# Kernel optimization log

Measured on AMD Instinct MI355X. Metric: run time of the kernel, lower is better.

The kernel has to match this reference:

```python
import jax, jax.numpy as jnp
import numpy as np

HIDDEN = 2048
KEY = 2048
EPS = 1e-05


def setup_inputs() -> dict:
    key = jax.random.key(0)
    k1, k2, k3 = jax.random.split(key, 3)
    B, S = 4, 2048
    x = jax.random.normal(k1, (B, S, HIDDEN), dtype=jnp.float32)
    # kaiming_uniform_ bound for fan_in=HIDDEN (a=sqrt(5) default): sqrt(6/((1+5)*fan_in)) = 1/sqrt(fan_in)
    bq = 1.0 / np.sqrt(HIDDEN)
    qkv = jax.random.uniform(k2, (HIDDEN, KEY * 3), minval=-bq, maxval=bq, dtype=jnp.float32)
    bo = 1.0 / np.sqrt(KEY)
    o_proj = jax.random.uniform(k3, (KEY, HIDDEN), minval=-bo, maxval=bo, dtype=jnp.float32)
    gamma = jnp.ones((HIDDEN,), dtype=jnp.float32)
    beta = jnp.zeros((HIDDEN,), dtype=jnp.float32)
    return {"x": x, "qkv": qkv, "o_proj": o_proj, "gamma": gamma, "beta": beta}


def reference(x, qkv, o_proj, gamma, beta):
    residual = x
    # LayerNorm over last dim
    mu = jnp.mean(x, axis=-1, keepdims=True)
    var = jnp.mean((x - mu) ** 2, axis=-1, keepdims=True)
    x_norm = (x - mu) / jnp.sqrt(var + EPS) * gamma + beta
    q = x_norm @ qkv[:, :KEY]          # [B,S,K]
    k = x_norm @ qkv[:, KEY:2 * KEY]   # [B,S,K]
    v = x_norm @ qkv[:, 2 * KEY:]      # [B,S,K]
    scale = 1.0 / jnp.sqrt(jnp.float32(KEY))
    scores = jnp.einsum('bsk,btk->bst', q, k) * scale  # [B,S,S]
    S_len = x.shape[1]
    causal = jnp.tril(jnp.ones((S_len, S_len), dtype=bool))
    scores = jnp.where(causal[None], scores, -jnp.inf)
    attn = jax.nn.softmax(scores, axis=-1)
    out = attn @ v          # [B,S,K]
    out = out @ o_proj      # [B,S,H]
    return out + residual
```

## Files before the change

### kernel.cpp

```cpp
#include <hip/hip_runtime.h>
#include <stdint.h>

typedef short short8 __attribute__((ext_vector_type(8)));
typedef unsigned short ushort8 __attribute__((ext_vector_type(8)));
typedef unsigned short ushort4v __attribute__((ext_vector_type(4)));
typedef float f32x4 __attribute__((ext_vector_type(4)));

#define HD 2048
#define S_LEN 2048
#define NROWS 8192
#define N3 6144

typedef __attribute__((address_space(3))) void lds_void_t;
typedef __attribute__((address_space(1))) void g_void_t;

__device__ inline void gload_lds16(const void* g, void* l) {
    __builtin_amdgcn_global_load_lds((g_void_t*)g, (lds_void_t*)l, 16, 0, 0);
}

__device__ inline unsigned short f2bf(float f) {
    unsigned u = __float_as_uint(f);
    unsigned r = (u + 0x7FFFu + ((u >> 16) & 1u)) >> 16;
    return (unsigned short)r;
}
__device__ inline float bf2f(unsigned short h) {
    return __uint_as_float(((unsigned)h) << 16);
}

__global__ __launch_bounds__(256) void ln_kernel(const float* __restrict__ x,
    const float* __restrict__ gamma, const float* __restrict__ beta,
    unsigned short* __restrict__ xn) {
    int row = blockIdx.x;
    const float* xr = x + (size_t)row * HD;
    int tid = threadIdx.x;
    float v[8];
    float4 a = *(const float4*)(xr + tid * 8);
    float4 b = *(const float4*)(xr + tid * 8 + 4);
    v[0]=a.x; v[1]=a.y; v[2]=a.z; v[3]=a.w; v[4]=b.x; v[5]=b.y; v[6]=b.z; v[7]=b.w;
    float s = 0.f, ss = 0.f;
#pragma unroll
    for (int e = 0; e < 8; e++) { s += v[e]; ss += v[e] * v[e]; }
    for (int off = 32; off > 0; off >>= 1) {
        s += __shfl_down(s, off);
        ss += __shfl_down(ss, off);
    }
    __shared__ float red[10];
    int wave = tid >> 6, lane = tid & 63;
    if (lane == 0) { red[wave] = s; red[4 + wave] = ss; }
    __syncthreads();
    if (tid == 0) {
        float S = red[0] + red[1] + red[2] + red[3];
        float SS = red[4] + red[5] + red[6] + red[7];
        float mu = S * (1.0f / HD);
        float var = SS * (1.0f / HD) - mu * mu;
        red[8] = mu;
        red[9] = rsqrtf(var + 1e-5f);
    }
    __syncthreads();
    float mu = red[8], rstd = red[9];
#pragma unroll
    for (int e = 0; e < 8; e++) {
        int c = tid * 8 + e;
        float val = (v[e] - mu) * rstd * gamma[c] + beta[c];
        xn[(size_t)row * HD + c] = f2bf(val);
    }
}

__global__ __launch_bounds__(256) void transp_f32_bf16(const float* __restrict__ src, int ld_s,
    unsigned short* __restrict__ dst, int ld_d) {
    __shared__ float tile[32][33];
    int c0 = blockIdx.x * 32, r0 = blockIdx.y * 32;
    int tc = threadIdx.x & 31, tr = threadIdx.x >> 5;
#pragma unroll
    for (int i = 0; i < 32; i += 8)
        tile[tr + i][tc] = src[(size_t)(r0 + tr + i) * ld_s + c0 + tc];
    __syncthreads();
#pragma unroll
    for (int i = 0; i < 32; i += 8)
        dst[(size_t)(c0 + tr + i) * ld_d + r0 + tc] = f2bf(tile[tc][tr + i]);
}

__global__ __launch_bounds__(256) void softmax_causal(unsigned short* __restrict__ sc) {
    int r = blockIdx.x;
    int s = r & (S_LEN - 1);
    unsigned short* row = sc + (size_t)r * S_LEN;
    int tid = threadIdx.x;
    ushort8 u = *(const ushort8*)(row + tid * 8);
    float v[8];
    float mx = -3.0e38f;
#pragma unroll
    for (int e = 0; e < 8; e++) {
        int t = tid * 8 + e;
        float f = bf2f(u[e]);
        v[e] = (t <= s) ? f : -3.0e38f;
        mx = fmaxf(mx, v[e]);
    }
    for (int off = 32; off > 0; off >>= 1) mx = fmaxf(mx, __shfl_down(mx, off));
    __shared__ float red[8];
    int wave = tid >> 6, lane = tid & 63;
    if (lane == 0) red[wave] = mx;
    __syncthreads();
    mx = fmaxf(fmaxf(red[0], red[1]), fmaxf(red[2], red[3]));
    float ex[8];
    float sum = 0.f;
#pragma unroll
    for (int e = 0; e < 8; e++) {
        ex[e] = (v[e] > -1.0e38f) ? __expf(v[e] - mx) : 0.f;
        sum += ex[e];
    }
    for (int off = 32; off > 0; off >>= 1) sum += __shfl_down(sum, off);
    if (lane == 0) red[4 + wave] = sum;
    __syncthreads();
    float inv = 1.0f / (red[4] + red[5] + red[6] + red[7]);
#pragma unroll
    for (int e = 0; e < 8; e++) {
        row[tid * 8 + e] = f2bf(ex[e] * inv);
    }
}

template <int EPI>
__global__ __launch_bounds__(256) void gemm_nt(
    const unsigned short* __restrict__ Ab, int lda, long sAz,
    const unsigned short* __restrict__ Bb, int ldb, long sBz,
    void* __restrict__ Cb, int ldc, long sCz,
    int kdim, int causal, float scale, const float* __restrict__ resid,
    unsigned short* __restrict__ vt) {
    int bx = blockIdx.x, by = blockIdx.y, bz = blockIdx.z;
    if (causal) by = gridDim.y - 1 - by;
    if (causal == 1 && bx > by) return;
    const unsigned short* A = Ab + (size_t)bz * sAz;
    const unsigned short* Bt = Bb + (size_t)bz * sBz;
    int kmax = kdim;
    if (causal == 2) { int km = (by + 1) * 128; if (km < kmax) kmax = km; }
    int m0 = by * 128, n0 = bx * 128;

    __shared__ unsigned short lA[128 * 64];
    __shared__ unsigned short lB[128 * 64];

    int tid = threadIdx.x;
    int wave = tid >> 6, lane = tid & 63;
    int quad = lane >> 4, l16 = lane & 15;
    int wr = wave >> 1, wc = wave & 1;

    int rstage = wave * 32 + (lane >> 2);
    int ck = (lane & 3) * 8;
    const unsigned short* gA[2][2];
    const unsigned short* gB[2][2];
    unsigned short* ldA[2][2];
    unsigned short* ldB[2][2];
#pragma unroll
    for (int r16 = 0; r16 < 2; r16++)
#pragma unroll
        for (int h = 0; h < 2; h++) {
            gA[r16][h] = A + (size_t)(m0 + rstage + r16 * 16) * lda + h * 32 + ck;
            gB[r16][h] = Bt + (size_t)(n0 + rstage + r16 * 16) * ldb + h * 32 + ck;
            ldA[r16][h] = &lA[h * 4096 + (wave * 32 + r16 * 16) * 32];
            ldB[r16][h] = &lB[h * 4096 + (wave * 32 + r16 * 16) * 32];
        }

    f32x4 acc[4][4] = {};

    for (int k0 = 0; k0 < kmax; k0 += 64) {
        __syncthreads();
#pragma unroll
        for (int r16 = 0; r16 < 2; r16++)
#pragma unroll
            for (int h = 0; h < 2; h++) {
                gload_lds16(gA[r16][h], ldA[r16][h]);
                gload_lds16(gB[r16][h], ldB[r16][h]);
            }
        __syncthreads();
#pragma unroll
        for (int h = 0; h < 2; h++) {
            short8 af[4], bfr[4];
#pragma unroll
            for (int i = 0; i < 4; i++)
                af[i] = *(const short8*)&lA[h * 4096 + (wr * 64 + i * 16 + l16) * 32 + quad * 8];
#pragma unroll
            for (int j = 0; j < 4; j++)
                bfr[j] = *(const short8*)&lB[h * 4096 + (wc * 64 + j * 16 + l16) * 32 + quad * 8];
#pragma unroll
            for (int i = 0; i < 4; i++)
#pragma unroll
                for (int j = 0; j < 4; j++)
                    acc[i][j] = __builtin_amdgcn_mfma_f32_16x16x32_bf16(af[i], bfr[j], acc[i][j], 0, 0, 0);
        }
#pragma unroll
        for (int r16 = 0; r16 < 2; r16++)
#pragma unroll
            for (int h = 0; h < 2; h++) { gA[r16][h] += 64; gB[r16][h] += 64; }
    }

    int row0 = m0 + wr * 64 + quad * 4;
    int col0 = n0 + wc * 64 + l16;
    if (EPI == 3 && n0 >= 4096) {
        int batch = m0 >> 11;
        int sl0 = (m0 & 2047) + wr * 64 + quad * 4;
#pragma unroll
        for (int j = 0; j < 4; j++) {
            int kcol = (n0 - 4096) + wc * 64 + j * 16 + l16;
            unsigned short* base = vt + (size_t)batch * S_LEN * S_LEN + (size_t)kcol * S_LEN + sl0;
#pragma unroll
            for (int i = 0; i < 4; i++) {
                ushort4v p;
#pragma unroll
                for (int r = 0; r < 4; r++) p[r] = f2bf(acc[i][j][r]);
                *(ushort4v*)(base + i * 16) = p;
            }
        }
    } else if (EPI == 0 || EPI == 1 || EPI == 3) {
        unsigned short* C = (unsigned short*)Cb + (size_t)bz * sCz;
#pragma unroll
        for (int i = 0; i < 4; i++)
#pragma unroll
            for (int r = 0; r < 4; r++) {
                int row = row0 + i * 16 + r;
#pragma unroll
                for (int j = 0; j < 4; j++) {
                    float v = acc[i][j][r];
                    if (EPI == 1) v *= scale;
                    C[(size_t)row * ldc + col0 + j * 16] = f2bf(v);
                }
            }
    } else {
        float* C = (float*)Cb + (size_t)bz * sCz;
#pragma unroll
        for (int i = 0; i < 4; i++)
#pragma unroll
            for (int r = 0; r < 4; r++) {
                int row = row0 + i * 16 + r;
#pragma unroll
                for (int j = 0; j < 4; j++) {
                    int col = col0 + j * 16;
                    C[(size_t)row * ldc + col] = acc[i][j][r] + resid[(size_t)row * ldc + col];
                }
            }
    }
}

extern "C" void kernel_launch(void* const* d_in, const int* in_sizes, int n_in,
                              void* d_out, int out_size, void* d_ws, size_t ws_size,
                              hipStream_t stream) {
    const float* x      = (const float*)d_in[0];
    const float* qkv    = (const float*)d_in[1];
    const float* o_proj = (const float*)d_in[2];
    const float* gamma  = (const float*)d_in[3];
    const float* beta   = (const float*)d_in[4];
    float* out = (float*)d_out;

    char* w = (char*)d_ws;
    unsigned short* xn      = (unsigned short*)(w);
    unsigned short* w_t     = (unsigned short*)(w + 33554432);
    unsigned short* o_t     = (unsigned short*)(w + 58720256);
    unsigned short* qkv_out = (unsigned short*)(w + 67108864);
    unsigned short* v_t     = (unsigned short*)(w + 167772160);
    unsigned short* scores  = xn;

    ln_kernel<<<NROWS, 256, 0, stream>>>(x, gamma, beta, xn);
    transp_f32_bf16<<<dim3(192, 64), 256, 0, stream>>>(qkv, N3, w_t, HD);
    transp_f32_bf16<<<dim3(64, 64), 256, 0, stream>>>(o_proj, HD, o_t, HD);
    gemm_nt<3><<<dim3(48, 64, 1), 256, 0, stream>>>(xn, HD, 0L, w_t, HD, 0L,
        (void*)qkv_out, N3, 0L, HD, 0, 1.0f, nullptr, v_t);
    float scale = 0.022097086912079608f;
    gemm_nt<1><<<dim3(16, 16, 4), 256, 0, stream>>>(qkv_out, N3, (long)S_LEN * N3,
        qkv_out + 2048, N3, (long)S_LEN * N3,
        (void*)scores, S_LEN, (long)S_LEN * S_LEN, HD, 1, scale, nullptr, nullptr);
    softmax_causal<<<NROWS, 256, 0, stream>>>(scores);
    gemm_nt<0><<<dim3(16, 16, 4), 256, 0, stream>>>(scores, S_LEN, (long)S_LEN * S_LEN,
        v_t, S_LEN, (long)HD * S_LEN,
        (void*)qkv_out, N3, (long)S_LEN * N3, S_LEN, 2, 1.0f, nullptr, nullptr);
    gemm_nt<2><<<dim3(16, 64, 1), 256, 0, stream>>>(qkv_out, N3, 0L, o_t, HD, 0L,
        (void*)out, HD, 0L, HD, 0, 1.0f, x, nullptr);
}
```

Before: 661.2 us.

## Add 256x256-tile GEMM with 4-stage LDS pipeline for QKV and output projections

Introduces a new GEMM kernel with 256x256 output tiles, 512 threads, a four-buffer LDS ring filled by direct global-to-LDS loads, split A/B staging interleaved with MFMA phases, and an XCD-aware block remap. It replaces the old 128-tile GEMM for the QKV projection and the output projection with residual add. Larger tiles raise arithmetic intensity and reduce global traffic, and the deeper pipeline hides load latency. In exchange it uses far more LDS and registers per block, and the output projection launches only 256 blocks, which may underfill the GPU.

After: 617.7 us. 1.07x faster.

```diff
diff --git a/kernel.cpp b/kernel.cpp
--- a/kernel.cpp
+++ b/kernel.cpp
@@ -238,6 +238,153 @@
     }
 }
 
+template <int EPI>
+__global__ __launch_bounds__(512, 2) void gemm256_nt(
+    const unsigned short* __restrict__ A, int lda,
+    const unsigned short* __restrict__ Bt, int ldb,
+    void* __restrict__ Cb, int ldc,
+    int kdim, int nbx,
+    const float* __restrict__ resid, unsigned short* __restrict__ vt) {
+
+    __shared__ unsigned short lds[4][2][8192];
+
+    unsigned id = blockIdx.x;
+    unsigned nwg = gridDim.x;
+    unsigned wg = (id & 7u) * (nwg >> 3) + (id >> 3);
+    int bx = (int)(wg % (unsigned)nbx), by = (int)(wg / (unsigned)nbx);
+    int m0 = by * 256, n0 = bx * 256;
+
+    int tid = threadIdx.x;
+    int wave = tid >> 6, lane = tid & 63;
+    int quad = lane >> 4, l16 = lane & 15;
+    int wr = wave >> 2, wc = wave & 3;
+
+    int laneoff = (l16 * 64 + quad * 16) ^ ((l16 & 7) << 4);
+
+    int q = tid >> 2;
+    int rsw = q ^ ((q >> 2) & 1);
+    int scol = ((tid & 3) ^ (rsw & 3)) << 3;
+    const unsigned short* gA0 = A + (size_t)(m0 + rsw) * lda + scol;
+    const unsigned short* gA1 = A + (size_t)(m0 + 128 + rsw) * lda + scol;
+    const unsigned short* gB0 = Bt + (size_t)(n0 + rsw) * ldb + scol;
+    const unsigned short* gB1 = Bt + (size_t)(n0 + 128 + rsw) * ldb + scol;
+
+    int nkt = kdim >> 5;
+
+#pragma unroll
+    for (int u = 0; u < 3; ++u) {
+        if (u < nkt) {
+            char* dA = (char*)&lds[u][0][0] + wave * 1024;
+            char* dB = (char*)&lds[u][1][0] + wave * 1024;
+            gload_lds16(gA0 + u * 32, dA);
+            gload_lds16(gA1 + u * 32, dA + 8192);
+            gload_lds16(gB0 + u * 32, dB);
+            gload_lds16(gB1 + u * 32, dB + 8192);
+        }
+    }
+    gA0 += 96; gA1 += 96; gB0 += 96; gB1 += 96;
+    if (nkt > 2)      asm volatile("s_waitcnt vmcnt(8)" ::: "memory");
+    else if (nkt > 1) asm volatile("s_waitcnt vmcnt(4)" ::: "memory");
+    else              asm volatile("s_waitcnt vmcnt(0)" ::: "memory");
+    __builtin_amdgcn_s_barrier();
+
+    f32x4 acc[8][4] = {};
+
+    for (int t = 0; t < nkt; ++t) {
+        int buf = t & 3, sbuf = (t + 3) & 3;
+        const char* lA = (const char*)&lds[buf][0][0];
+        const char* lB = (const char*)&lds[buf][1][0];
+        bool do_stage = (t + 3 < nkt);
+
+        short8 af[4], bfr[4];
+#pragma unroll
+        for (int i = 0; i < 4; ++i)
+            af[i] = *(const short8*)(lA + wr * 8192 + i * 1024 + laneoff);
+#pragma unroll
+        for (int j = 0; j < 4; ++j)
+            bfr[j] = *(const short8*)(lB + wc * 4096 + j * 1024 + laneoff);
+        if (do_stage) {
+            char* dA = (char*)&lds[sbuf][0][0] + wave * 1024;
+            gload_lds16(gA0, dA);
+            gload_lds16(gA1, dA + 8192);
+        }
+        __builtin_amdgcn_s_barrier();
+        __builtin_amdgcn_s_setprio(1);
+#pragma unroll
+        for (int i = 0; i < 4; ++i)
+#pragma unroll
+            for (int j = 0; j < 4; ++j)
+                acc[i][j] = __builtin_amdgcn_mfma_f32_16x16x32_bf16(af[i], bfr[j], acc[i][j], 0, 0, 0);
+        __builtin_amdgcn_s_setprio(0);
+        __builtin_amdgcn_s_barrier();
+
+        short8 ag[4];
+#pragma unroll
+        for (int i = 0; i < 4; ++i)
+            ag[i] = *(const short8*)(lA + wr * 8192 + (4 + i) * 1024 + laneoff);
+        if (do_stage) {
+            char* dB = (char*)&lds[sbuf][1][0] + wave * 1024;
+            gload_lds16(gB0, dB);
+            gload_lds16(gB1, dB + 8192);
+        }
+        if (t + 3 < nkt)      asm volatile("s_waitcnt vmcnt(8)" ::: "memory");
+        else if (t + 2 < nkt) asm volatile("s_waitcnt vmcnt(4)" ::: "memory");
+        else if (t + 1 < nkt) asm volatile("s_waitcnt vmcnt(0)" ::: "memory");
+        __builtin_amdgcn_s_barrier();
+        __builtin_amdgcn_s_setprio(1);
+#pragma unroll
+        for (int i = 0; i < 4; ++i)
+#pragma unroll
+            for (int j = 0; j < 4; ++j)
+                acc[4 + i][j] = __builtin_amdgcn_mfma_f32_16x16x32_bf16(ag[i], bfr[j], acc[4 + i][j], 0, 0, 0);
+        __builtin_amdgcn_s_setprio(0);
+        __builtin_amdgcn_s_barrier();
+
+        gA0 += 32; gA1 += 32; gB0 += 32; gB1 += 32;
+    }
+
+    if (EPI == 3 && n0 >= 4096) {
+        int batch = m0 >> 11;
+        int sl0 = (m0 & 2047) + wr * 128 + quad * 4;
+#pragma unroll
+        for (int j = 0; j < 4; ++j) {
+            int kcol = (n0 - 4096) + wc * 64 + j * 16 + l16;
+            unsigned short* base = vt + (size_t)batch * S_LEN * S_LEN + (size_t)kcol * S_LEN + sl0;
+#pragma unroll
+            for (int i = 0; i < 8; ++i) {
+                ushort4v p;
+#pragma unroll
+                for (int r = 0; r < 4; ++r) p[r] = f2bf(acc[i][j][r]);
+                *(ushort4v*)(base + i * 16) = p;
+            }
+        }
+    } else if (EPI == 3) {
+        unsigned short* C = (unsigned short*)Cb;
+#pragma unroll
+        for (int i = 0; i < 8; ++i)
+#pragma unroll
+            for (int r = 0; r < 4; ++r) {
+                int row = m0 + wr * 128 + i * 16 + quad * 4 + r;
+#pragma unroll
+                for (int j = 0; j < 4; ++j)
+                    C[(size_t)row * ldc + n0 + wc * 64 + j * 16 + l16] = f2bf(acc[i][j][r]);
+            }
+    } else {
+        float* C = (float*)Cb;
+#pragma unroll
+        for (int i = 0; i < 8; ++i)
+#pragma unroll
+            for (int r = 0; r < 4; ++r) {
+                int row = m0 + wr * 128 + i * 16 + quad * 4 + r;
+#pragma unroll
+                for (int j = 0; j < 4; ++j) {
+                    int col = n0 + wc * 64 + j * 16 + l16;
+                    C[(size_t)row * ldc + col] = acc[i][j][r] + resid[(size_t)row * ldc + col];
+                }
+            }
+    }
+}
+
 extern "C" void kernel_launch(void* const* d_in, const int* in_sizes, int n_in,
                               void* d_out, int out_size, void* d_ws, size_t ws_size,
                               hipStream_t stream) {
@@ -259,8 +406,8 @@
     ln_kernel<<<NROWS, 256, 0, stream>>>(x, gamma, beta, xn);
     transp_f32_bf16<<<dim3(192, 64), 256, 0, stream>>>(qkv, N3, w_t, HD);
     transp_f32_bf16<<<dim3(64, 64), 256, 0, stream>>>(o_proj, HD, o_t, HD);
-    gemm_nt<3><<<dim3(48, 64, 1), 256, 0, stream>>>(xn, HD, 0L, w_t, HD, 0L,
-        (void*)qkv_out, N3, 0L, HD, 0, 1.0f, nullptr, v_t);
+    gemm256_nt<3><<<dim3(768), 512, 0, stream>>>(xn, HD, w_t, HD,
+        (void*)qkv_out, N3, HD, 24, nullptr, v_t);
     float scale = 0.022097086912079608f;
     gemm_nt<1><<<dim3(16, 16, 4), 256, 0, stream>>>(qkv_out, N3, (long)S_LEN * N3,
         qkv_out + 2048, N3, (long)S_LEN * N3,
@@ -269,6 +416,6 @@
     gemm_nt<0><<<dim3(16, 16, 4), 256, 0, stream>>>(scores, S_LEN, (long)S_LEN * S_LEN,
         v_t, S_LEN, (long)HD * S_LEN,
         (void*)qkv_out, N3, (long)S_LEN * N3, S_LEN, 2, 1.0f, nullptr, nullptr);
-    gemm_nt<2><<<dim3(16, 64, 1), 256, 0, stream>>>(qkv_out, N3, 0L, o_t, HD, 0L,
-        (void*)out, HD, 0L, HD, 0, 1.0f, x, nullptr);
-}
+    gemm256_nt<2><<<dim3(256), 512, 0, stream>>>(qkv_out, N3, o_t, HD,
+        (void*)out, HD, HD, 8, x, nullptr);
+}
```
